# Kernel tuning notes

Hardware: AMD Instinct MI355X
Metric: run time of the kernel (lower is better)

The kernel has to match this reference:

```python
import jax, jax.numpy as jnp
import numpy as np

N = 50000      # nodes
E = 600000     # edges
D_IN = 128
D_H = 128
D_OUT = 64


def setup_inputs() -> dict:
    key = jax.random.key(0)
    ks = jax.random.split(key, 10)
    x = jax.random.normal(ks[0], (N, D_IN), dtype=jnp.float32)
    edge_index = jax.random.randint(ks[1], (2, E), 0, N, dtype=jnp.int32)
    def lin(k, fan_out, fan_in):
        s = 1.0 / np.sqrt(fan_in)
        return jax.random.uniform(k, (fan_out, fan_in), jnp.float32, -s, s)
    W0 = lin(ks[2], D_H, D_IN);   b0 = jnp.zeros((D_H,), jnp.float32)
    W1 = lin(ks[3], D_H, D_H);    b1 = jnp.zeros((D_H,), jnp.float32)
    W2 = lin(ks[4], D_H, D_H);    b2 = jnp.zeros((D_H,), jnp.float32)
    W3 = lin(ks[5], D_OUT, D_H);  b3 = jnp.zeros((D_OUT,), jnp.float32)
    return {"x": x, "edge_index": edge_index,
            "W0": W0, "b0": b0, "W1": W1, "b1": b1,
            "W2": W2, "b2": b2, "W3": W3, "b3": b3}


def reference(x, edge_index, W0, b0, W1, b1, W2, b2, W3, b3):
    n = x.shape[0]
    loops = jnp.arange(n, dtype=edge_index.dtype)
    row = jnp.concatenate([edge_index[0], loops])  # sources (with self-loops)
    col = jnp.concatenate([edge_index[1], loops])  # targets
    # symmetric normalization D^-1/2 (A+I) D^-1/2 (PyG GCNConv default)
    deg = jax.ops.segment_sum(jnp.ones(row.shape, x.dtype), col, num_segments=n)
    dinv = jnp.where(deg > 0, jax.lax.rsqrt(deg), 0.0)
    norm = dinv[row] * dinv[col]  # [E+N]

    def gcn_conv(h, W, b):
        h = h @ W.T                              # [n, out]
        msg = h[row] * norm[:, None]             # gather + scale
        out = jax.ops.segment_sum(msg, col, num_segments=n)  # scatter-add
        return out + b

    h = jax.nn.relu(gcn_conv(x, W0, b0))   # Dropout is identity in eval mode
    h = jax.nn.relu(gcn_conv(h, W1, b1))
    h = jax.nn.relu(gcn_conv(h, W2, b2))
    return gcn_conv(h, W3, b3)
```

## Files before the change

kernel.cpp:

```cpp
#include <hip/hip_runtime.h>

#define D_INF 128
#define D_HF  128
#define D_OUTF 64

typedef __attribute__((ext_vector_type(8))) short bf16x8;
typedef __attribute__((ext_vector_type(4))) float f32x4;
typedef unsigned short u16;
typedef unsigned int   u32;

__device__ inline u16 f2bf(float f) {
    u32 u = __float_as_uint(f);
    u32 r = (u + 0x7fffu + ((u >> 16) & 1u)) >> 16;
    return (u16)r;
}
__device__ inline float bf2f(u16 h) { return __uint_as_float(((u32)h) << 16); }

__global__ void k_zero_i32(int* p, int n) {
    int i = blockIdx.x * blockDim.x + threadIdx.x;
    if (i < n) p[i] = 0;
}

__global__ void k_count(const int* __restrict__ colv, int* __restrict__ cnt, int E) {
    int e = blockIdx.x * blockDim.x + threadIdx.x;
    if (e < E) atomicAdd(&cnt[colv[e]], 1);
}

__global__ void k_dinv_from_cnt(const int* __restrict__ cnt, float* __restrict__ dinv, int n) {
    int i = blockIdx.x * blockDim.x + threadIdx.x;
    if (i < n) dinv[i] = (float)(1.0 / sqrt((double)(cnt[i] + 1)));
}

__global__ void k_scan_block(const int* __restrict__ cnt, int* __restrict__ rp,
                             int* __restrict__ bsum, int n) {
    __shared__ int sm[256];
    int t = threadIdx.x;
    int i = blockIdx.x * 256 + t;
    int v = (i < n) ? cnt[i] : 0;
    sm[t] = v;
    __syncthreads();
    for (int off = 1; off < 256; off <<= 1) {
        int x = sm[t];
        int y = (t >= off) ? sm[t - off] : 0;
        __syncthreads();
        sm[t] = x + y;
        __syncthreads();
    }
    if (i < n) rp[i] = sm[t] - v;
    if (t == 255) bsum[blockIdx.x] = sm[t];
}

__global__ void k_scan_bsum(int* __restrict__ bsum, int nb) {
    __shared__ int sm[256];
    int t = threadIdx.x;
    int v = (t < nb) ? bsum[t] : 0;
    sm[t] = v;
    __syncthreads();
    for (int off = 1; off < 256; off <<= 1) {
        int x = sm[t];
        int y = (t >= off) ? sm[t - off] : 0;
        __syncthreads();
        sm[t] = x + y;
        __syncthreads();
    }
    if (t < nb) bsum[t] = sm[t] - v;
}

__global__ void k_scan_add2(int* __restrict__ rp, const int* __restrict__ bsum, int n) {
    int i = blockIdx.x * 256 + threadIdx.x;
    if (i < n) rp[i] += bsum[blockIdx.x];
}

__global__ void k_scatter(const int* __restrict__ row, const int* __restrict__ colv,
                          const float* __restrict__ dinv, const int* __restrict__ rp,
                          int* __restrict__ fill, int* __restrict__ csr_src,
                          float* __restrict__ csr_w, int E) {
    int e = blockIdx.x * blockDim.x + threadIdx.x;
    if (e >= E) return;
    int r = row[e], c = colv[e];
    int pos = rp[c] + atomicAdd(&fill[c], 1);
    csr_src[pos] = r;
    csr_w[pos] = dinv[r] * dinv[c];
}

__global__ void k_split_x(const float* __restrict__ x, u16* __restrict__ Xcat,
                          int Nreal, int Mpad) {
    int idx = blockIdx.x * 256 + threadIdx.x;
    int total = Mpad * 32;
    if (idx >= total) return;
    const int row = idx >> 5, c4 = (idx & 31) * 4;
    float4 v = make_float4(0.f, 0.f, 0.f, 0.f);
    if (row < Nreal) v = *(const float4*)(x + (size_t)row * 128 + c4);
    u16 h0 = f2bf(v.x), h1 = f2bf(v.y), h2 = f2bf(v.z), h3 = f2bf(v.w);
    u16 l0 = f2bf(v.x - bf2f(h0)), l1 = f2bf(v.y - bf2f(h1));
    u16 l2 = f2bf(v.z - bf2f(h2)), l3 = f2bf(v.w - bf2f(h3));
    u16* dst = Xcat + (size_t)row * 256 + c4;
    *(u32*)(dst)       = (u32)h0 | ((u32)h1 << 16);
    *(u32*)(dst + 2)   = (u32)h2 | ((u32)h3 << 16);
    *(u32*)(dst + 128) = (u32)l0 | ((u32)l1 << 16);
    *(u32*)(dst + 130) = (u32)l2 | ((u32)l3 << 16);
}

__global__ void k_split_w(const float* __restrict__ W0, const float* __restrict__ W1,
                          const float* __restrict__ W2, const float* __restrict__ W3,
                          u16* __restrict__ Wcat) {
    const int l = blockIdx.y;
    const float* W = (l == 0) ? W0 : (l == 1) ? W1 : (l == 2) ? W2 : W3;
    const int rows = (l == 3) ? 64 : 128;
    int idx = blockIdx.x * 256 + threadIdx.x;
    if (idx >= rows * 128) return;
    const int r = idx >> 7, c = idx & 127;
    float v = W[idx];
    u16 h = f2bf(v);
    u16 lo = f2bf(v - bf2f(h));
    u16* dst = Wcat + (size_t)l * 128 * 256 + (size_t)r * 256 + c;
    dst[0]   = h;
    dst[128] = lo;
}

template <int FM>
__global__ __launch_bounds__(256)
void k_gemm_mfma(const u16* __restrict__ Xcat, const u16* __restrict__ Wcat,
                 float* __restrict__ H) {
    constexpr int Dout = (FM == 4) ? 128 : 64;
    const int tid = threadIdx.x;
    const int wave = tid >> 6, lane = tid & 63;
    const int wm = (FM == 4) ? (wave >> 1) : wave;
    const int wn = (FM == 4) ? (wave & 1) : 0;
    const int row_base = blockIdx.x * 128 + wm * (FM * 16);
    const int col_base = wn * 64;
    const int lr = lane & 15;
    const int kg = lane >> 4;

    f32x4 acc[FM][4] = {};

    #pragma unroll 2
    for (int ks = 0; ks < 8; ++ks) {
        const int k0 = ks * 32 + kg * 8;
        bf16x8 a[FM], b[4];
        #pragma unroll
        for (int i = 0; i < FM; ++i)
            a[i] = *(const bf16x8*)(Xcat + (size_t)(row_base + i * 16 + lr) * 256 + k0);
        #pragma unroll
        for (int j = 0; j < 4; ++j)
            b[j] = *(const bf16x8*)(Wcat + (size_t)(col_base + j * 16 + lr) * 256 + k0);
        #pragma unroll
        for (int i = 0; i < FM; ++i)
            #pragma unroll
            for (int j = 0; j < 4; ++j)
                acc[i][j] = __builtin_amdgcn_mfma_f32_16x16x32_bf16(a[i], b[j], acc[i][j], 0, 0, 0);
    }

    #pragma unroll
    for (int i = 0; i < FM; ++i) {
        const int r0 = row_base + i * 16 + kg * 4;
        #pragma unroll
        for (int j = 0; j < 4; ++j) {
            const int c = col_base + j * 16 + lr;
            #pragma unroll
            for (int q = 0; q < 4; ++q)
                H[(size_t)(r0 + q) * Dout + c] = acc[i][j][q];
        }
    }
}

template <int D, int OUT_MODE>
__global__ void k_agg_gather(const float* __restrict__ H, const float* __restrict__ dinv,
                             const int* __restrict__ rp, const int* __restrict__ csr_src,
                             const float* __restrict__ csr_w, const float* __restrict__ b,
                             void* __restrict__ out, int N, int E) {
    const int node = blockIdx.x * 4 + (threadIdx.x >> 6);
    const int lane = threadIdx.x & 63;
    if (node >= N) return;
    const int beg = rp[node];
    const int end = (node == N - 1) ? E : rp[node + 1];
    const int deg = end - beg;
    const float di = dinv[node];
    const double wself = (double)di * (double)di;

    if (D == 128) {
        const int d0 = lane * 2;
        double a0[8] = {}, a1[8] = {};
        {
            const float2 hs = *(const float2*)(H + (size_t)node * D + d0);
            a0[0] = wself * hs.x; a1[0] = wself * hs.y;
        }
        for (int base = 0; base < deg; base += 64) {
            const int m = min(64, deg - base);
            int s_l = 0; float w_l = 0.f;
            if (lane < m) {
                s_l = csr_src[beg + base + lane];
                w_l = csr_w[beg + base + lane];
            }
            int j = 0;
            for (; j + 8 <= m; j += 8) {
                int s[8]; float w[8];
                #pragma unroll
                for (int q = 0; q < 8; ++q) {
                    s[q] = __shfl(s_l, j + q);
                    w[q] = __shfl(w_l, j + q);
                }
                float2 h[8];
                #pragma unroll
                for (int q = 0; q < 8; ++q)
                    h[q] = *(const float2*)(H + (size_t)s[q] * D + d0);
                #pragma unroll
                for (int q = 0; q < 8; ++q) {
                    a0[q] += (double)w[q] * h[q].x;
                    a1[q] += (double)w[q] * h[q].y;
                }
            }
            for (; j < m; ++j) {
                const int s = __shfl(s_l, j);
                const float w = __shfl(w_l, j);
                const float2 hv = *(const float2*)(H + (size_t)s * D + d0);
                a0[0] += (double)w * hv.x; a1[0] += (double)w * hv.y;
            }
        }
        double A0 = ((a0[0] + a0[1]) + (a0[2] + a0[3])) + ((a0[4] + a0[5]) + (a0[6] + a0[7]));
        double A1 = ((a1[0] + a1[1]) + (a1[2] + a1[3])) + ((a1[4] + a1[5]) + (a1[6] + a1[7]));
        float v0 = (float)(A0 + (double)b[d0]);
        float v1 = (float)(A1 + (double)b[d0 + 1]);
        if (OUT_MODE == 1) {
            v0 = fmaxf(v0, 0.0f); v1 = fmaxf(v1, 0.0f);
            const u16 h0 = f2bf(v0), h1 = f2bf(v1);
            const u16 l0 = f2bf(v0 - bf2f(h0)), l1 = f2bf(v1 - bf2f(h1));
            u16* xc = (u16*)out + (size_t)node * 256 + d0;
            *(u32*)(xc)       = (u32)h0 | ((u32)h1 << 16);
            *(u32*)(xc + 128) = (u32)l0 | ((u32)l1 << 16);
        } else {
            *(float2*)((float*)out + (size_t)node * D + d0) = make_float2(v0, v1);
        }
    } else {
        const int half = lane >> 5;
        const int l32 = lane & 31;
        const int d0 = l32 * 2;
        double a0[4] = {}, a1[4] = {};
        if (half == 0) {
            const float2 hs = *(const float2*)(H + (size_t)node * D + d0);
            a0[0] = wself * hs.x; a1[0] = wself * hs.y;
        }
        for (int base = 0; base < deg; base += 64) {
            const int m = min(64, deg - base);
            int s_l = 0; float w_l = 0.f;
            if (lane < m) {
                s_l = csr_src[beg + base + lane];
                w_l = csr_w[beg + base + lane];
            }
            int j = 0;
            for (; j + 8 <= m; j += 8) {
                int s[4]; float w[4];
                #pragma unroll
                for (int q = 0; q < 4; ++q) {
                    s[q] = __shfl(s_l, j + 2 * q + half);
                    w[q] = __shfl(w_l, j + 2 * q + half);
                }
                float2 h[4];
                #pragma unroll
                for (int q = 0; q < 4; ++q)
                    h[q] = *(const float2*)(H + (size_t)s[q] * D + d0);
                #pragma unroll
                for (int q = 0; q < 4; ++q) {
                    a0[q] += (double)w[q] * h[q].x;
                    a1[q] += (double)w[q] * h[q].y;
                }
            }
            for (; j < m; j += 2) {
                const int e = j + half;
                if (e < m) {
                    const int s = __shfl(s_l, e);
                    const float w = __shfl(w_l, e);
                    const float2 hv = *(const float2*)(H + (size_t)s * D + d0);
                    a0[0] += (double)w * hv.x; a1[0] += (double)w * hv.y;
                }
            }
        }
        double A0 = (a0[0] + a0[1]) + (a0[2] + a0[3]);
        double A1 = (a1[0] + a1[1]) + (a1[2] + a1[3]);
        A0 += __shfl_xor(A0, 32);
        A1 += __shfl_xor(A1, 32);
        if (half == 0) {
            float v0 = (float)(A0 + (double)b[d0]);
            float v1 = (float)(A1 + (double)b[d0 + 1]);
            *(float2*)((float*)out + (size_t)node * D + d0) = make_float2(v0, v1);
        }
    }
}

extern "C" void kernel_launch(void* const* d_in, const int* in_sizes, int n_in,
                              void* d_out, int out_size, void* d_ws, size_t ws_size,
                              hipStream_t stream) {
    const float* x  = (const float*)d_in[0];
    const int*   ei = (const int*)d_in[1];
    const float* W[4] = {(const float*)d_in[2], (const float*)d_in[4],
                         (const float*)d_in[6], (const float*)d_in[8]};
    const float* B[4] = {(const float*)d_in[3], (const float*)d_in[5],
                         (const float*)d_in[7], (const float*)d_in[9]};
    const int N = in_sizes[0] / D_INF;
    const int E = in_sizes[1] / 2;
    const int Mpad = (N + 127) & ~127;
    const int* row  = ei;
    const int* colv = ei + E;

    size_t nPad = ((size_t)N + 255) & ~(size_t)255;
    size_t ePad = ((size_t)E + 255) & ~(size_t)255;
    float* dinv    = (float*)d_ws;
    int*   cnt     = (int*)(dinv + nPad);
    int*   bsum    = cnt + nPad;
    int*   rp      = bsum + 256;
    int*   csr_src = rp + nPad;
    float* csr_w   = (float*)(csr_src + ePad);
    float* Hbuf    = csr_w + ePad;
    u16*   Xcat    = (u16*)(Hbuf + (size_t)Mpad * 128);
    u16*   Wcat    = Xcat + (size_t)Mpad * 256;

    const int TB = 256;
    int nbN = (N + TB - 1) / TB;
    int nbE = (E + TB - 1) / TB;

    k_zero_i32<<<nbN, TB, 0, stream>>>(cnt, N);
    k_count<<<nbE, TB, 0, stream>>>(colv, cnt, E);
    k_dinv_from_cnt<<<nbN, TB, 0, stream>>>(cnt, dinv, N);
    k_scan_block<<<nbN, TB, 0, stream>>>(cnt, rp, bsum, N);
    k_scan_bsum<<<1, 256, 0, stream>>>(bsum, nbN);
    k_scan_add2<<<nbN, TB, 0, stream>>>(rp, bsum, N);
    k_zero_i32<<<nbN, TB, 0, stream>>>(cnt, N);
    k_scatter<<<nbE, TB, 0, stream>>>(row, colv, dinv, rp, cnt, csr_src, csr_w, E);

    k_split_x<<<(Mpad * 32 + TB - 1) / TB, TB, 0, stream>>>(x, Xcat, N, Mpad);
    {
        dim3 g(64, 4);
        k_split_w<<<g, TB, 0, stream>>>(W[0], W[1], W[2], W[3], Wcat);
    }

    const int aggGrid = (N + 3) / 4;
    const int gemmGrid = Mpad / 128;

    for (int l = 0; l < 3; ++l) {
        k_gemm_mfma<4><<<gemmGrid, 256, 0, stream>>>(Xcat, Wcat + (size_t)l * 128 * 256, Hbuf);
        k_agg_gather<128, 1><<<aggGrid, TB, 0, stream>>>(Hbuf, dinv, rp, csr_src, csr_w,
                                                         B[l], (void*)Xcat, N, E);
    }
    k_gemm_mfma<2><<<gemmGrid, 256, 0, stream>>>(Xcat, Wcat + (size_t)3 * 128 * 256, Hbuf);
    k_agg_gather<64, 0><<<aggGrid, TB, 0, stream>>>(Hbuf, dinv, rp, csr_src, csr_w,
                                                    B[3], d_out, N, E);
}
```

Before: 336.5 us.

## Fuse dinv and counter reset into scan; unroll gather by 16 without tails

The degree-to-dinv computation and the second counter zeroing are folded into the block scan kernel, which removes two small kernel launches from the preprocessing chain. The aggregation gather loops now process edges in padded groups of 16 with no scalar tail loop. Out-of-range lanes shuffle index 0 with weight 0, so each padded slot issues a real load of row 0. This buys more memory-level parallelism per wave at the cost of extra register pressure and some wasted loads on low-degree nodes.

```diff
diff --git a/kernel.cpp b/kernel.cpp
--- a/kernel.cpp
+++ b/kernel.cpp
@@ -26,13 +26,8 @@
     if (e < E) atomicAdd(&cnt[colv[e]], 1);
 }
 
-__global__ void k_dinv_from_cnt(const int* __restrict__ cnt, float* __restrict__ dinv, int n) {
-    int i = blockIdx.x * blockDim.x + threadIdx.x;
-    if (i < n) dinv[i] = (float)(1.0 / sqrt((double)(cnt[i] + 1)));
-}
-
-__global__ void k_scan_block(const int* __restrict__ cnt, int* __restrict__ rp,
-                             int* __restrict__ bsum, int n) {
+__global__ void k_scan_block(int* __restrict__ cnt, int* __restrict__ rp,
+                             int* __restrict__ bsum, float* __restrict__ dinv, int n) {
     __shared__ int sm[256];
     int t = threadIdx.x;
     int i = blockIdx.x * 256 + t;
@@ -46,7 +41,11 @@
         sm[t] = x + y;
         __syncthreads();
     }
-    if (i < n) rp[i] = sm[t] - v;
+    if (i < n) {
+        rp[i] = sm[t] - v;
+        dinv[i] = (float)(1.0 / sqrt((double)(v + 1)));
+        cnt[i] = 0;
+    }
     if (t == 255) bsum[blockIdx.x] = sm[t];
 }
 
@@ -192,29 +191,23 @@
                 s_l = csr_src[beg + base + lane];
                 w_l = csr_w[beg + base + lane];
             }
-            int j = 0;
-            for (; j + 8 <= m; j += 8) {
-                int s[8]; float w[8];
-                #pragma unroll
-                for (int q = 0; q < 8; ++q) {
+            const int m16 = (m + 15) & ~15;
+            for (int j = 0; j < m16; j += 16) {
+                int s[16]; float w[16];
+                #pragma unroll
+                for (int q = 0; q < 16; ++q) {
                     s[q] = __shfl(s_l, j + q);
                     w[q] = __shfl(w_l, j + q);
                 }
-                float2 h[8];
-                #pragma unroll
-                for (int q = 0; q < 8; ++q)
+                float2 h[16];
+                #pragma unroll
+                for (int q = 0; q < 16; ++q)
                     h[q] = *(const float2*)(H + (size_t)s[q] * D + d0);
                 #pragma unroll
-                for (int q = 0; q < 8; ++q) {
-                    a0[q] += (double)w[q] * h[q].x;
-                    a1[q] += (double)w[q] * h[q].y;
+                for (int q = 0; q < 16; ++q) {
+                    a0[q & 7] += (double)w[q] * h[q].x;
+                    a1[q & 7] += (double)w[q] * h[q].y;
                 }
-            }
-            for (; j < m; ++j) {
-                const int s = __shfl(s_l, j);
-                const float w = __shfl(w_l, j);
-                const float2 hv = *(const float2*)(H + (size_t)s * D + d0);
-                a0[0] += (double)w * hv.x; a1[0] += (double)w * hv.y;
             }
         }
         double A0 = ((a0[0] + a0[1]) + (a0[2] + a0[3])) + ((a0[4] + a0[5]) + (a0[6] + a0[7]));
@@ -235,7 +228,7 @@
         const int half = lane >> 5;
         const int l32 = lane & 31;
         const int d0 = l32 * 2;
-        double a0[4] = {}, a1[4] = {};
+        double a0[8] = {}, a1[8] = {};
         if (half == 0) {
             const float2 hs = *(const float2*)(H + (size_t)node * D + d0);
             a0[0] = wself * hs.x; a1[0] = wself * hs.y;
@@ -247,36 +240,28 @@
                 s_l = csr_src[beg + base + lane];
                 w_l = csr_w[beg + base + lane];
             }
-            int j = 0;
-            for (; j + 8 <= m; j += 8) {
-                int s[4]; float w[4];
-                #pragma unroll
-                for (int q = 0; q < 4; ++q) {
-                    s[q] = __shfl(s_l, j + 2 * q + half);
-                    w[q] = __shfl(w_l, j + 2 * q + half);
+            const int m16 = (m + 15) & ~15;
+            for (int j = 0; j < m16; j += 16) {
+                int s[8]; float w[8];
+                #pragma unroll
+                for (int q = 0; q < 8; ++q) {
+                    const int e = j + 2 * q + half;
+                    s[q] = __shfl(s_l, e);
+                    w[q] = __shfl(w_l, e);
                 }
-                float2 h[4];
-                #pragma unroll
-                for (int q = 0; q < 4; ++q)
+                float2 h[8];
+                #pragma unroll
+                for (int q = 0; q < 8; ++q)
                     h[q] = *(const float2*)(H + (size_t)s[q] * D + d0);
                 #pragma unroll
-                for (int q = 0; q < 4; ++q) {
+                for (int q = 0; q < 8; ++q) {
                     a0[q] += (double)w[q] * h[q].x;
                     a1[q] += (double)w[q] * h[q].y;
                 }
             }
-            for (; j < m; j += 2) {
-                const int e = j + half;
-                if (e < m) {
-                    const int s = __shfl(s_l, e);
-                    const float w = __shfl(w_l, e);
-                    const float2 hv = *(const float2*)(H + (size_t)s * D + d0);
-                    a0[0] += (double)w * hv.x; a1[0] += (double)w * hv.y;
-                }
-            }
-        }
-        double A0 = (a0[0] + a0[1]) + (a0[2] + a0[3]);
-        double A1 = (a1[0] + a1[1]) + (a1[2] + a1[3]);
+        }
+        double A0 = ((a0[0] + a0[1]) + (a0[2] + a0[3])) + ((a0[4] + a0[5]) + (a0[6] + a0[7]));
+        double A1 = ((a1[0] + a1[1]) + (a1[2] + a1[3])) + ((a1[4] + a1[5]) + (a1[6] + a1[7]));
         A0 += __shfl_xor(A0, 32);
         A1 += __shfl_xor(A1, 32);
         if (half == 0) {
@@ -320,11 +305,9 @@
 
     k_zero_i32<<<nbN, TB, 0, stream>>>(cnt, N);
     k_count<<<nbE, TB, 0, stream>>>(colv, cnt, E);
-    k_dinv_from_cnt<<<nbN, TB, 0, stream>>>(cnt, dinv, N);
-    k_scan_block<<<nbN, TB, 0, stream>>>(cnt, rp, bsum, N);
+    k_scan_block<<<nbN, TB, 0, stream>>>(cnt, rp, bsum, dinv, N);
     k_scan_bsum<<<1, 256, 0, stream>>>(bsum, nbN);
     k_scan_add2<<<nbN, TB, 0, stream>>>(rp, bsum, N);
-    k_zero_i32<<<nbN, TB, 0, stream>>>(cnt, N);
     k_scatter<<<nbE, TB, 0, stream>>>(row, colv, dinv, rp, cnt, csr_src, csr_w, E);
 
     k_split_x<<<(Mpad * 32 + TB - 1) / TB, TB, 0, stream>>>(x, Xcat, N, Mpad);
```

Measured after the change: 331.9 us. No clear change (-1.4%).
